# Performance work log

Measured on AMD Instinct MI355X. Metric: run time of the kernel, lower is better.

The kernel has to match this reference:

```python
import jax, jax.numpy as jnp
import numpy as np

NUM_HEAD = 32
SIZE_PER_HEAD = 64
START_LEN = 4080
SEQ_LEN = 4096
STEPS = SEQ_LEN - START_LEN  # 16 unrolled decode steps
BATCH = 32
SCALE = 0.125  # hard-coded in the original (1/sqrt(64))


def setup_inputs() -> dict:
    key = jax.random.key(0)
    ks = jax.random.split(key, 7)
    B, H, D, S = BATCH, NUM_HEAD, SIZE_PER_HEAD, SEQ_LEN
    xavier = float(np.sqrt(6.0 / (D + D)))  # xavier_uniform_ bound for [D, D] fan
    return {
        "x": jax.random.normal(ks[0], (B, H, 1, D), dtype=jnp.float32),
        "k": jax.random.normal(ks[1], (B, H, S, D), dtype=jnp.float32),
        "v": jax.random.normal(ks[2], (B, H, S, D), dtype=jnp.float32),
        "wq": jax.random.uniform(ks[3], (H, D, D), jnp.float32, -xavier, xavier),
        "wk": jax.random.uniform(ks[4], (H, D, D), jnp.float32, -xavier, xavier),
        "wv": jax.random.uniform(ks[5], (H, D, D), jnp.float32, -xavier, xavier),
        "wo": jax.random.uniform(ks[6], (H, D, D), jnp.float32, -xavier, xavier),
    }


def _decode(x, k, v, wq, wk, wv, wo):
    # x: [B, H, 1, D]; k, v: [B, H, S, D]; weights: [H, D, D]
    def step(carry, _):
        x, k, v, gen_id = carry
        q = jnp.einsum("bhod,hde->bhoe", x, wq)            # [B, H, 1, D]
        k_new = jnp.einsum("bhod,hde->bhoe", x, wk)        # [B, H, 1, D]
        v_new = jnp.einsum("bhod,hde->bhoe", x, wv)
        k = jax.lax.dynamic_update_slice_in_dim(k, k_new, gen_id, axis=2)
        v = jax.lax.dynamic_update_slice_in_dim(v, v_new, gen_id, axis=2)
        # scores over the FULL cache (no mask), matching torch softmax over dim=3
        attn = jnp.einsum("bhsd,bhod->bhos", k, q) * SCALE  # [B, H, 1, S]
        attn = jax.nn.softmax(attn, axis=-1)
        x = jnp.einsum("bhos,bhsd->bhod", attn, v)          # [B, H, 1, D]
        x = jnp.einsum("bhod,hde->bhoe", x, wo)
        return (x, k, v, gen_id + 1), None

    (x, k, v, _), _ = jax.lax.scan(step, (x, k, v, jnp.int32(START_LEN)), None, length=STEPS)
    return x


def reference(x, k, v, wq, wk, wv, wo):
    return _decode(x, k, v, wq, wk, wv, wo)
```

## Files before the change

kernel.cpp:

```cpp
#include <hip/hip_runtime.h>
#include <hip/hip_fp16.h>
#include <math.h>

#define BATCH   32
#define NHEAD   32
#define DIM     64
#define SEQ     4096
#define START   4080
#define NSTEPS  16
#define SCALE   0.125f

template <bool USE_WS>
__launch_bounds__(256, 4)
__global__ void attn_unroll_kernel(const float* __restrict__ x_in,
                                   const float* __restrict__ k_in,
                                   const float* __restrict__ v_in,
                                   const float* __restrict__ wq,
                                   const float* __restrict__ wk,
                                   const float* __restrict__ wv,
                                   const float* __restrict__ wo,
                                   float* __restrict__ out,
                                   __half* __restrict__ kh_ws,
                                   __half* __restrict__ vh_ws)
{
    const int bid = blockIdx.x;
    const int h   = bid & (NHEAD - 1);
    const int tid = threadIdx.x;

    __shared__ float s_scores[SEQ];
    __shared__ float s_kext[NSTEPS][DIM];
    __shared__ float s_vext[NSTEPS][DIM];
    __shared__ float s_x[DIM];
    __shared__ float s_q[DIM];
    __shared__ float s_attn[DIM];
    __shared__ float s_red[4][DIM];
    __shared__ float s_wred[4];

    const float* __restrict__ K  = k_in + (size_t)bid * SEQ * DIM;
    const float* __restrict__ V  = v_in + (size_t)bid * SEQ * DIM;
    const float* __restrict__ Wq = wq + (size_t)h * DIM * DIM;
    const float* __restrict__ Wk = wk + (size_t)h * DIM * DIM;
    const float* __restrict__ Wv = wv + (size_t)h * DIM * DIM;
    const float* __restrict__ Wo = wo + (size_t)h * DIM * DIM;
    __half* __restrict__ Kh = USE_WS ? kh_ws + (size_t)bid * START * DIM : nullptr;
    __half* __restrict__ Vh = USE_WS ? vh_ws + (size_t)bid * START * DIM : nullptr;

    if (tid < DIM) s_x[tid] = x_in[(size_t)bid * DIM + tid];
    for (int i = tid; i < NSTEPS * DIM; i += 256) {
        (&s_kext[0][0])[i] = K[(size_t)START * DIM + i];
        (&s_vext[0][0])[i] = V[(size_t)START * DIM + i];
    }
    __syncthreads();

    auto project = [&](const float* in_vec, const float* __restrict__ W,
                       float* out_vec) {
        const int e = tid & 63;
        const int g = tid >> 6;
        float p = 0.f;
        #pragma unroll
        for (int dd = 0; dd < 16; ++dd) {
            const int d0 = g * 16 + dd;
            p += in_vec[d0] * W[d0 * 64 + e];
        }
        s_red[g][e] = p;
        __syncthreads();
        if (tid < 64)
            out_vec[tid] = s_red[0][tid] + s_red[1][tid]
                         + s_red[2][tid] + s_red[3][tid];
        __syncthreads();
    };

    const int c    = tid & 15;
    const int sr   = tid >> 4;
    const int c8   = tid & 7;
    const int rg   = tid >> 3;
    const int wave = tid >> 6;

    auto qk_f32 = [&]() {
        const float q0 = s_q[c * 4 + 0], q1 = s_q[c * 4 + 1];
        const float q2 = s_q[c * 4 + 2], q3 = s_q[c * 4 + 3];
        const float4* __restrict__ K4 = (const float4*)K;
        for (int it = 0; it < START / 16; ++it) {
            const int s = it * 16 + sr;
            const float4 kv = K4[s * 16 + c];
            if (USE_WS) {
                __half2* dst = (__half2*)(Kh + (size_t)s * DIM + c * 4);
                dst[0] = __floats2half2_rn(kv.x, kv.y);
                dst[1] = __floats2half2_rn(kv.z, kv.w);
            }
            float p = kv.x * q0 + kv.y * q1 + kv.z * q2 + kv.w * q3;
            p += __shfl_xor(p, 1);
            p += __shfl_xor(p, 2);
            p += __shfl_xor(p, 4);
            p += __shfl_xor(p, 8);
            if (c == 0) s_scores[s] = p;
        }
        {
            const int s = START + sr;
            const float* kr = s_kext[sr];
            float p = kr[c * 4 + 0] * q0 + kr[c * 4 + 1] * q1
                    + kr[c * 4 + 2] * q2 + kr[c * 4 + 3] * q3;
            p += __shfl_xor(p, 1);
            p += __shfl_xor(p, 2);
            p += __shfl_xor(p, 4);
            p += __shfl_xor(p, 8);
            if (c == 0) s_scores[s] = p;
        }
    };

    auto qk_h = [&]() {
        float qv[8];
        #pragma unroll
        for (int j = 0; j < 8; ++j) qv[j] = s_q[c8 * 8 + j];
        const float4* __restrict__ Kh4 = (const float4*)Kh;
        for (int it = 0; it < (START + 31) / 32; ++it) {
            const int s = it * 32 + rg;
            if (s < START) {
                float4 raw = Kh4[(size_t)s * 8 + c8];
                const __half2* hp = (const __half2*)&raw;
                float p = 0.f;
                #pragma unroll
                for (int j = 0; j < 4; ++j) {
                    const float2 f = __half22float2(hp[j]);
                    p += f.x * qv[2 * j] + f.y * qv[2 * j + 1];
                }
                p += __shfl_xor(p, 1);
                p += __shfl_xor(p, 2);
                p += __shfl_xor(p, 4);
                if (c8 == 0) s_scores[s] = p;
            }
        }
        if (tid < NSTEPS * 8) {
            const float* kr = s_kext[rg];
            float p = 0.f;
            #pragma unroll
            for (int j = 0; j < 8; ++j) p += kr[c8 * 8 + j] * qv[j];
            p += __shfl_xor(p, 1);
            p += __shfl_xor(p, 2);
            p += __shfl_xor(p, 4);
            if (c8 == 0) s_scores[START + rg] = p;
        }
    };

    auto pv_f32 = [&](float inv_total) {
        float ax = 0.f, ay = 0.f, az = 0.f, aw = 0.f;
        const float4* __restrict__ V4 = (const float4*)V;
        for (int it = 0; it < START / 16; ++it) {
            const int s = it * 16 + sr;
            const float a  = s_scores[s];
            const float4 vv = V4[s * 16 + c];
            if (USE_WS) {
                __half2* dst = (__half2*)(Vh + (size_t)s * DIM + c * 4);
                dst[0] = __floats2half2_rn(vv.x, vv.y);
                dst[1] = __floats2half2_rn(vv.z, vv.w);
            }
            ax += a * vv.x; ay += a * vv.y; az += a * vv.z; aw += a * vv.w;
        }
        {
            const int s = START + sr;
            const float a  = s_scores[s];
            const float* vr = s_vext[sr];
            ax += a * vr[c * 4 + 0]; ay += a * vr[c * 4 + 1];
            az += a * vr[c * 4 + 2]; aw += a * vr[c * 4 + 3];
        }
        ax += __shfl_xor(ax, 16); ax += __shfl_xor(ax, 32);
        ay += __shfl_xor(ay, 16); ay += __shfl_xor(ay, 32);
        az += __shfl_xor(az, 16); az += __shfl_xor(az, 32);
        aw += __shfl_xor(aw, 16); aw += __shfl_xor(aw, 32);
        if ((tid & 63) < 16) {
            s_red[wave][c * 4 + 0] = ax;
            s_red[wave][c * 4 + 1] = ay;
            s_red[wave][c * 4 + 2] = az;
            s_red[wave][c * 4 + 3] = aw;
        }
        __syncthreads();
        if (tid < 64)
            s_attn[tid] = (s_red[0][tid] + s_red[1][tid]
                         + s_red[2][tid] + s_red[3][tid]) * inv_total;
        __syncthreads();
    };

    auto pv_h = [&](float inv_total) {
        float a[8];
        #pragma unroll
        for (int j = 0; j < 8; ++j) a[j] = 0.f;
        const float4* __restrict__ Vh4 = (const float4*)Vh;
        for (int it = 0; it < (START + 31) / 32; ++it) {
            const int s = it * 32 + rg;
            if (s < START) {
                const float w = s_scores[s];
                float4 raw = Vh4[(size_t)s * 8 + c8];
                const __half2* hp = (const __half2*)&raw;
                #pragma unroll
                for (int j = 0; j < 4; ++j) {
                    const float2 f = __half22float2(hp[j]);
                    a[2 * j + 0] += w * f.x;
                    a[2 * j + 1] += w * f.y;
                }
            }
        }
        if (tid < NSTEPS * 8) {
            const float w = s_scores[START + rg];
            const float* vr = s_vext[rg];
            #pragma unroll
            for (int j = 0; j < 8; ++j) a[j] += w * vr[c8 * 8 + j];
        }
        #pragma unroll
        for (int j = 0; j < 8; ++j) {
            a[j] += __shfl_xor(a[j], 8);
            a[j] += __shfl_xor(a[j], 16);
            a[j] += __shfl_xor(a[j], 32);
        }
        if ((tid & 63) < 8) {
            #pragma unroll
            for (int j = 0; j < 8; ++j) s_red[wave][c8 * 8 + j] = a[j];
        }
        __syncthreads();
        if (tid < 64)
            s_attn[tid] = (s_red[0][tid] + s_red[1][tid]
                         + s_red[2][tid] + s_red[3][tid]) * inv_total;
        __syncthreads();
    };

    for (int step = 0; step < NSTEPS; ++step) {
        project(s_x, Wq, s_q);
        project(s_x, Wk, s_kext[step]);
        project(s_x, Wv, s_vext[step]);
        if (tid < 64) s_q[tid] *= SCALE;
        __syncthreads();

        if (USE_WS && step > 0) qk_h(); else qk_f32();
        __syncthreads();

        float lmax = -1e30f;
        #pragma unroll
        for (int i = 0; i < 16; ++i)
            lmax = fmaxf(lmax, s_scores[tid + i * 256]);
        #pragma unroll
        for (int off = 1; off < 64; off <<= 1)
            lmax = fmaxf(lmax, __shfl_xor(lmax, off));
        if ((tid & 63) == 0) s_wred[wave] = lmax;
        __syncthreads();
        const float bmax = fmaxf(fmaxf(s_wred[0], s_wred[1]),
                                 fmaxf(s_wred[2], s_wred[3]));
        float lsum = 0.f;
        #pragma unroll
        for (int i = 0; i < 16; ++i) {
            const float e = __expf(s_scores[tid + i * 256] - bmax);
            s_scores[tid + i * 256] = e;
            lsum += e;
        }
        #pragma unroll
        for (int off = 1; off < 64; off <<= 1)
            lsum += __shfl_xor(lsum, off);
        __syncthreads();
        if ((tid & 63) == 0) s_wred[wave] = lsum;
        __syncthreads();
        const float inv_total = 1.f / (s_wred[0] + s_wred[1]
                                     + s_wred[2] + s_wred[3]);

        if (USE_WS && step > 0) pv_h(inv_total); else pv_f32(inv_total);

        project(s_attn, Wo, s_x);
    }

    if (tid < 64) out[(size_t)bid * DIM + tid] = s_x[tid];
}

extern "C" void kernel_launch(void* const* d_in, const int* in_sizes, int n_in,
                              void* d_out, int out_size, void* d_ws, size_t ws_size,
                              hipStream_t stream) {
    const float* x  = (const float*)d_in[0];
    const float* k  = (const float*)d_in[1];
    const float* v  = (const float*)d_in[2];
    const float* wq = (const float*)d_in[3];
    const float* wk = (const float*)d_in[4];
    const float* wv = (const float*)d_in[5];
    const float* wo = (const float*)d_in[6];
    float* out = (float*)d_out;

    const size_t half_elems = (size_t)BATCH * NHEAD * START * DIM;
    const size_t need = 2 * half_elems * sizeof(__half);

    if (ws_size >= need) {
        __half* kh = (__half*)d_ws;
        __half* vh = kh + half_elems;
        attn_unroll_kernel<true><<<BATCH * NHEAD, 256, 0, stream>>>(
            x, k, v, wq, wk, wv, wo, out, kh, vh);
    } else {
        attn_unroll_kernel<false><<<BATCH * NHEAD, 256, 0, stream>>>(
            x, k, v, wq, wk, wv, wo, out, nullptr, nullptr);
    }
}
```

Measured before the change: 3.584 ms.

## Use 512-thread blocks with padded LDS and nontemporal fp32 K/V loads

Doubles the threads per block to 512 and rewrites the score, softmax, PV and projection loops and reductions for 8 waves. Adds a dummy dynamic LDS allocation so that only one block fits per CU. The first-step fp32 K/V streaming reads become nontemporal loads. The goal is shorter per-block sequential steps and less cache pollution, at the cost of fewer concurrent blocks per CU and more block-wide synchronisation.

```diff
diff --git a/kernel.cpp b/kernel.cpp
--- a/kernel.cpp
+++ b/kernel.cpp
@@ -9,9 +9,13 @@
 #define START   4080
 #define NSTEPS  16
 #define SCALE   0.125f
+#define NTHR    512
+#define DYN_LDS 57344
+
+typedef float fvec4 __attribute__((ext_vector_type(4)));
 
 template <bool USE_WS>
-__launch_bounds__(256, 4)
+__launch_bounds__(NTHR, 1)
 __global__ void attn_unroll_kernel(const float* __restrict__ x_in,
                                    const float* __restrict__ k_in,
                                    const float* __restrict__ v_in,
@@ -23,6 +27,9 @@
                                    __half* __restrict__ kh_ws,
                                    __half* __restrict__ vh_ws)
 {
+    extern __shared__ float s_pad[];
+    (void)s_pad;
+
     const int bid = blockIdx.x;
     const int h   = bid & (NHEAD - 1);
     const int tid = threadIdx.x;
@@ -33,8 +40,8 @@
     __shared__ float s_x[DIM];
     __shared__ float s_q[DIM];
     __shared__ float s_attn[DIM];
-    __shared__ float s_red[4][DIM];
-    __shared__ float s_wred[4];
+    __shared__ float s_red[8][DIM];
+    __shared__ float s_wred[8];
 
     const float* __restrict__ K  = k_in + (size_t)bid * SEQ * DIM;
     const float* __restrict__ V  = v_in + (size_t)bid * SEQ * DIM;
@@ -46,7 +53,7 @@
     __half* __restrict__ Vh = USE_WS ? vh_ws + (size_t)bid * START * DIM : nullptr;
 
     if (tid < DIM) s_x[tid] = x_in[(size_t)bid * DIM + tid];
-    for (int i = tid; i < NSTEPS * DIM; i += 256) {
+    for (int i = tid; i < NSTEPS * DIM; i += NTHR) {
         (&s_kext[0][0])[i] = K[(size_t)START * DIM + i];
         (&s_vext[0][0])[i] = V[(size_t)START * DIM + i];
     }
@@ -58,15 +65,18 @@
         const int g = tid >> 6;
         float p = 0.f;
         #pragma unroll
-        for (int dd = 0; dd < 16; ++dd) {
-            const int d0 = g * 16 + dd;
+        for (int dd = 0; dd < 8; ++dd) {
+            const int d0 = g * 8 + dd;
             p += in_vec[d0] * W[d0 * 64 + e];
         }
         s_red[g][e] = p;
         __syncthreads();
-        if (tid < 64)
-            out_vec[tid] = s_red[0][tid] + s_red[1][tid]
-                         + s_red[2][tid] + s_red[3][tid];
+        if (tid < 64) {
+            float r = 0.f;
+            #pragma unroll
+            for (int w = 0; w < 8; ++w) r += s_red[w][tid];
+            out_vec[tid] = r;
+        }
         __syncthreads();
     };
 
@@ -79,10 +89,8 @@
     auto qk_f32 = [&]() {
         const float q0 = s_q[c * 4 + 0], q1 = s_q[c * 4 + 1];
         const float q2 = s_q[c * 4 + 2], q3 = s_q[c * 4 + 3];
-        const float4* __restrict__ K4 = (const float4*)K;
-        for (int it = 0; it < START / 16; ++it) {
-            const int s = it * 16 + sr;
-            const float4 kv = K4[s * 16 + c];
+        const fvec4* __restrict__ K4 = (const fvec4*)K;
+        auto row = [&](int s, fvec4 kv) {
             if (USE_WS) {
                 __half2* dst = (__half2*)(Kh + (size_t)s * DIM + c * 4);
                 dst[0] = __floats2half2_rn(kv.x, kv.y);
@@ -94,8 +102,16 @@
             p += __shfl_xor(p, 4);
             p += __shfl_xor(p, 8);
             if (c == 0) s_scores[s] = p;
-        }
-        {
+        };
+        for (int it = 0; it < 127; ++it) {
+            const int s = it * 32 + sr;
+            row(s, __builtin_nontemporal_load(&K4[s * 16 + c]));
+        }
+        if (sr < 16) {
+            const int s = 4064 + sr;
+            row(s, __builtin_nontemporal_load(&K4[s * 16 + c]));
+        }
+        if (sr < 16) {
             const int s = START + sr;
             const float* kr = s_kext[sr];
             float p = kr[c * 4 + 0] * q0 + kr[c * 4 + 1] * q1
@@ -112,25 +128,26 @@
         float qv[8];
         #pragma unroll
         for (int j = 0; j < 8; ++j) qv[j] = s_q[c8 * 8 + j];
-        const float4* __restrict__ Kh4 = (const float4*)Kh;
-        for (int it = 0; it < (START + 31) / 32; ++it) {
-            const int s = it * 32 + rg;
-            if (s < START) {
-                float4 raw = Kh4[(size_t)s * 8 + c8];
-                const __half2* hp = (const __half2*)&raw;
-                float p = 0.f;
-                #pragma unroll
-                for (int j = 0; j < 4; ++j) {
-                    const float2 f = __half22float2(hp[j]);
-                    p += f.x * qv[2 * j] + f.y * qv[2 * j + 1];
-                }
-                p += __shfl_xor(p, 1);
-                p += __shfl_xor(p, 2);
-                p += __shfl_xor(p, 4);
-                if (c8 == 0) s_scores[s] = p;
+        const fvec4* __restrict__ Kh4 = (const fvec4*)Kh;
+        auto row = [&](int s) {
+            fvec4 raw = Kh4[(size_t)s * 8 + c8];
+            const __half2* hp = (const __half2*)&raw;
+            float p = 0.f;
+            #pragma unroll
+            for (int j = 0; j < 4; ++j) {
+                const float2 f = __half22float2(hp[j]);
+                p += f.x * qv[2 * j] + f.y * qv[2 * j + 1];
             }
-        }
-        if (tid < NSTEPS * 8) {
+            p += __shfl_xor(p, 1);
+            p += __shfl_xor(p, 2);
+            p += __shfl_xor(p, 4);
+            if (c8 == 0) s_scores[s] = p;
+        };
+        for (int it = 0; it < 63; ++it)
+            row(it * 64 + rg);
+        if (rg < 48)
+            row(4032 + rg);
+        if (rg < 16) {
             const float* kr = s_kext[rg];
             float p = 0.f;
             #pragma unroll
@@ -144,19 +161,25 @@
 
     auto pv_f32 = [&](float inv_total) {
         float ax = 0.f, ay = 0.f, az = 0.f, aw = 0.f;
-        const float4* __restrict__ V4 = (const float4*)V;
-        for (int it = 0; it < START / 16; ++it) {
-            const int s = it * 16 + sr;
-            const float a  = s_scores[s];
-            const float4 vv = V4[s * 16 + c];
+        const fvec4* __restrict__ V4 = (const fvec4*)V;
+        auto row = [&](int s, fvec4 vv) {
             if (USE_WS) {
                 __half2* dst = (__half2*)(Vh + (size_t)s * DIM + c * 4);
                 dst[0] = __floats2half2_rn(vv.x, vv.y);
                 dst[1] = __floats2half2_rn(vv.z, vv.w);
             }
+            const float a = s_scores[s];
             ax += a * vv.x; ay += a * vv.y; az += a * vv.z; aw += a * vv.w;
-        }
-        {
+        };
+        for (int it = 0; it < 127; ++it) {
+            const int s = it * 32 + sr;
+            row(s, __builtin_nontemporal_load(&V4[s * 16 + c]));
+        }
+        if (sr < 16) {
+            const int s = 4064 + sr;
+            row(s, __builtin_nontemporal_load(&V4[s * 16 + c]));
+        }
+        if (sr < 16) {
             const int s = START + sr;
             const float a  = s_scores[s];
             const float* vr = s_vext[sr];
@@ -174,9 +197,12 @@
             s_red[wave][c * 4 + 3] = aw;
         }
         __syncthreads();
-        if (tid < 64)
-            s_attn[tid] = (s_red[0][tid] + s_red[1][tid]
-                         + s_red[2][tid] + s_red[3][tid]) * inv_total;
+        if (tid < 64) {
+            float r = 0.f;
+            #pragma unroll
+            for (int w = 0; w < 8; ++w) r += s_red[w][tid];
+            s_attn[tid] = r * inv_total;
+        }
         __syncthreads();
     };
 
@@ -184,22 +210,23 @@
         float a[8];
         #pragma unroll
         for (int j = 0; j < 8; ++j) a[j] = 0.f;
-        const float4* __restrict__ Vh4 = (const float4*)Vh;
-        for (int it = 0; it < (START + 31) / 32; ++it) {
-            const int s = it * 32 + rg;
-            if (s < START) {
-                const float w = s_scores[s];
-                float4 raw = Vh4[(size_t)s * 8 + c8];
-                const __half2* hp = (const __half2*)&raw;
-                #pragma unroll
-                for (int j = 0; j < 4; ++j) {
-                    const float2 f = __half22float2(hp[j]);
-                    a[2 * j + 0] += w * f.x;
-                    a[2 * j + 1] += w * f.y;
-                }
+        const fvec4* __restrict__ Vh4 = (const fvec4*)Vh;
+        auto row = [&](int s) {
+            const float w = s_scores[s];
+            fvec4 raw = Vh4[(size_t)s * 8 + c8];
+            const __half2* hp = (const __half2*)&raw;
+            #pragma unroll
+            for (int j = 0; j < 4; ++j) {
+                const float2 f = __half22float2(hp[j]);
+                a[2 * j + 0] += w * f.x;
+                a[2 * j + 1] += w * f.y;
             }
-        }
-        if (tid < NSTEPS * 8) {
+        };
+        for (int it = 0; it < 63; ++it)
+            row(it * 64 + rg);
+        if (rg < 48)
+            row(4032 + rg);
+        if (rg < 16) {
             const float w = s_scores[START + rg];
             const float* vr = s_vext[rg];
             #pragma unroll
@@ -216,9 +243,12 @@
             for (int j = 0; j < 8; ++j) s_red[wave][c8 * 8 + j] = a[j];
         }
         __syncthreads();
-        if (tid < 64)
-            s_attn[tid] = (s_red[0][tid] + s_red[1][tid]
-                         + s_red[2][tid] + s_red[3][tid]) * inv_total;
+        if (tid < 64) {
+            float r = 0.f;
+            #pragma unroll
+            for (int w = 0; w < 8; ++w) r += s_red[w][tid];
+            s_attn[tid] = r * inv_total;
+        }
         __syncthreads();
     };
 
@@ -234,20 +264,21 @@
 
         float lmax = -1e30f;
         #pragma unroll
-        for (int i = 0; i < 16; ++i)
-            lmax = fmaxf(lmax, s_scores[tid + i * 256]);
+        for (int i = 0; i < 8; ++i)
+            lmax = fmaxf(lmax, s_scores[tid + i * NTHR]);
         #pragma unroll
         for (int off = 1; off < 64; off <<= 1)
             lmax = fmaxf(lmax, __shfl_xor(lmax, off));
         if ((tid & 63) == 0) s_wred[wave] = lmax;
         __syncthreads();
-        const float bmax = fmaxf(fmaxf(s_wred[0], s_wred[1]),
-                                 fmaxf(s_wred[2], s_wred[3]));
+        float bmax = s_wred[0];
+        #pragma unroll
+        for (int w = 1; w < 8; ++w) bmax = fmaxf(bmax, s_wred[w]);
         float lsum = 0.f;
         #pragma unroll
-        for (int i = 0; i < 16; ++i) {
-            const float e = __expf(s_scores[tid + i * 256] - bmax);
-            s_scores[tid + i * 256] = e;
+        for (int i = 0; i < 8; ++i) {
+            const float e = __expf(s_scores[tid + i * NTHR] - bmax);
+            s_scores[tid + i * NTHR] = e;
             lsum += e;
         }
         #pragma unroll
@@ -256,8 +287,10 @@
         __syncthreads();
         if ((tid & 63) == 0) s_wred[wave] = lsum;
         __syncthreads();
-        const float inv_total = 1.f / (s_wred[0] + s_wred[1]
-                                     + s_wred[2] + s_wred[3]);
+        float tot = 0.f;
+        #pragma unroll
+        for (int w = 0; w < 8; ++w) tot += s_wred[w];
+        const float inv_total = 1.f / tot;
 
         if (USE_WS && step > 0) pv_h(inv_total); else pv_f32(inv_total);
 
@@ -285,10 +318,10 @@
     if (ws_size >= need) {
         __half* kh = (__half*)d_ws;
         __half* vh = kh + half_elems;
-        attn_unroll_kernel<true><<<BATCH * NHEAD, 256, 0, stream>>>(
+        attn_unroll_kernel<true><<<BATCH * NHEAD, NTHR, DYN_LDS, stream>>>(
             x, k, v, wq, wk, wv, wo, out, kh, vh);
     } else {
-        attn_unroll_kernel<false><<<BATCH * NHEAD, 256, 0, stream>>>(
+        attn_unroll_kernel<false><<<BATCH * NHEAD, NTHR, DYN_LDS, stream>>>(
             x, k, v, wq, wk, wv, wo, out, nullptr, nullptr);
     }
 }
```

Measured after the change: 4.083 ms. +13.9%, slower.
